# Performance work log

Hardware: AMD Instinct MI355X
Metric: run time of the kernel (lower is better)

The kernel has to match this reference:

```python
import jax, jax.numpy as jnp
import numpy as np

KERNEL_MUL = 2.0
KERNEL_NUM = 5
EPS = 1e-8


def _l2_normalize(x):
    # F.normalize(p=2, dim=-1): x / max(||x||, 1e-12)
    norm = jnp.sqrt(jnp.sum(x * x, axis=-1, keepdims=True))
    return x / jnp.maximum(norm, 1e-12)


def _mmd(source, target):
    n_s = source.shape[0]
    n_t = target.shape[0]
    s = _l2_normalize(source)
    t = _l2_normalize(target)
    total = jnp.concatenate([s, t], axis=0)  # [n, d]
    n = n_s + n_t
    # pairwise squared L2 via norm-expansion trick (avoids [n,n,d] intermediate)
    sq = jnp.sum(total * total, axis=-1)  # [n]
    gram = total @ total.T                # [n, n]
    d2 = jnp.maximum(sq[:, None] + sq[None, :] - 2.0 * gram, 0.0)
    # bandwidth from detached distances (torch uses .data)
    d2_ng = jax.lax.stop_gradient(d2)
    bandwidth = jnp.sum(d2_ng) / (n * n - n) + EPS
    bandwidth = bandwidth / (KERNEL_MUL ** (KERNEL_NUM // 2))
    kernels = jnp.zeros_like(d2)
    for i in range(KERNEL_NUM):
        kernels = kernels + jnp.exp(-d2 / (bandwidth * KERNEL_MUL ** i))
    XX = kernels[:n_s, :n_s]
    YY = kernels[n_s:, n_s:]
    XY = kernels[:n_s, n_s:]
    loss = (jnp.sum(XX) - jnp.trace(XX)) / (n_s * (n_s - 1))
    loss = loss + (jnp.sum(YY) - jnp.trace(YY)) / (n_t * (n_t - 1))
    loss = loss - 2.0 * jnp.sum(XY) / (n_s * n_t)
    return loss


def setup_inputs() -> dict:
    key = jax.random.key(0)
    k1, k2 = jax.random.split(key)
    source = jax.random.normal(k1, (4096, 512), dtype=jnp.float32)
    target = jax.random.normal(k2, (4096, 512), dtype=jnp.float32)
    return {"source": source, "target": target}


def reference(source, target):
    return _mmd(source, target)
```

## Files before the change

### kernel.cpp

```cpp
#include <hip/hip_runtime.h>

#define D 512
#define NS 4096
#define NROWS 8192
#define TILES 32
#define T_SYM 528
#define NBLK_GEMM (2 * T_SYM + TILES * TILES)

typedef __attribute__((ext_vector_type(8))) short bf16x8;
typedef __attribute__((ext_vector_type(4))) float f32x4;

__device__ __forceinline__ unsigned short f2bf(float f) {
  unsigned int u = __float_as_uint(f);
  u += 0x7fffu + ((u >> 16) & 1u);
  return (unsigned short)(u >> 16);
}
__device__ __forceinline__ float bf2f(unsigned short h) {
  return __uint_as_float(((unsigned int)h) << 16);
}
__device__ __forceinline__ void gload_lds16(const void* g, void* l) {
  __builtin_amdgcn_global_load_lds(
      (const __attribute__((address_space(1))) unsigned int*)g,
      (__attribute__((address_space(3))) unsigned int*)l, 16, 0, 0);
}

__global__ __launch_bounds__(256) void k_rownorm(const float* __restrict__ src,
                                                 const float* __restrict__ tgt,
                                                 float* __restrict__ sq,
                                                 unsigned short* __restrict__ hi,
                                                 unsigned short* __restrict__ lo,
                                                 float* __restrict__ colsum) {
  int t = threadIdx.x, w = t >> 6, l = t & 63;
  float csum[8] = {0.f, 0.f, 0.f, 0.f, 0.f, 0.f, 0.f, 0.f};
  for (int i = 0; i < 8; ++i) {
    int r = blockIdx.x * 32 + w * 8 + i;
    const float* p = (r < NS) ? (src + (size_t)r * D) : (tgt + (size_t)(r - NS) * D);
    float4 v0 = *(const float4*)(p + l * 8);
    float4 v1 = *(const float4*)(p + l * 8 + 4);
    float x[8] = {v0.x, v0.y, v0.z, v0.w, v1.x, v1.y, v1.z, v1.w};
    float s = 0.f;
    #pragma unroll
    for (int j = 0; j < 8; ++j) s += x[j] * x[j];
    #pragma unroll
    for (int off = 1; off < 64; off <<= 1) s += __shfl_xor(s, off);
    float iv = 1.0f / fmaxf(sqrtf(s), 1e-12f);
    if (l == 0) sq[r] = s * iv * iv;
    unsigned short hs[8], ls[8];
    #pragma unroll
    for (int j = 0; j < 8; ++j) {
      float xn = x[j] * iv;
      unsigned short h = f2bf(xn);
      hs[j] = h;
      ls[j] = f2bf(xn - bf2f(h));
      csum[j] += xn;
    }
    *(uint4*)&hi[(size_t)r * D + l * 8] = *(uint4*)hs;
    *(uint4*)&lo[(size_t)r * D + l * 8] = *(uint4*)ls;
  }
  __shared__ float cs[4][512];
  #pragma unroll
  for (int j = 0; j < 8; ++j) cs[w][l * 8 + j] = csum[j];
  __syncthreads();
  for (int c = t; c < 512; c += 256)
    atomicAdd(&colsum[c], cs[0][c] + cs[1][c] + cs[2][c] + cs[3][c]);
}

__global__ __launch_bounds__(256) void k_prep(const float* __restrict__ sq,
                                              const float* __restrict__ colsum,
                                              float* __restrict__ na) {
  int t = threadIdx.x;
  double ssq = 0.0;
  for (int i = t; i < NROWS; i += 256) ssq += (double)sq[i];
  double ss2 = 0.0;
  for (int c = t; c < D; c += 256) { double v = (double)colsum[c]; ss2 += v * v; }
  #pragma unroll
  for (int off = 32; off; off >>= 1) {
    ssq += __shfl_down(ssq, off);
    ss2 += __shfl_down(ss2, off);
  }
  __shared__ double l1[4], l2[4];
  if ((t & 63) == 0) { l1[t >> 6] = ssq; l2[t >> 6] = ss2; }
  __syncthreads();
  if (t == 0) {
    double SSQ = l1[0] + l1[1] + l1[2] + l1[3];
    double SS2 = l2[0] + l2[1] + l2[2] + l2[3];
    double n = (double)NROWS;
    double sum_d2 = 2.0 * n * SSQ - 2.0 * SS2;
    double bw = sum_d2 / (n * n - n) + 1e-8;
    bw = bw * 0.25;
    const double LOG2E = 1.4426950408889634;
    na[0] = (float)(-LOG2E / (bw * 16.0));
  }
}

__global__ __launch_bounds__(256) void k_gemm(const unsigned short* __restrict__ hi,
                                              const unsigned short* __restrict__ lo,
                                              const float* __restrict__ sq,
                                              const float* __restrict__ na,
                                              double* __restrict__ part) {
  __shared__ unsigned short lds[2 * 16384];
  __shared__ double red[4];

  int bid0 = blockIdx.x;
  int bid = (bid0 & 7) * (NBLK_GEMM / 8) + (bid0 >> 3);
  int type, bi, bj;
  float wgt = 1.f;
  if (bid < 2 * T_SYM) {
    type = (bid >= T_SYM);
    int idx = bid - type * T_SYM;
    bi = 0;
    while (idx >= TILES - bi) { idx -= TILES - bi; ++bi; }
    bj = bi + idx;
    wgt = (bi == bj) ? 1.f : 2.f;
  } else {
    type = 2;
    int rem = bid - 2 * T_SYM;
    bi = rem >> 5;
    bj = rem & 31;
  }
  int offA = (type == 1) ? NS : 0;
  int offB = (type == 0) ? 0 : NS;

  int t = threadIdx.x;
  int w = t >> 6, l = t & 63;
  int wr = w >> 1, wc = w & 1;
  int fr = l & 15, fk = l >> 4;

  const unsigned short* sarr = (w & 1) ? lo : hi;
  int rbase = ((w < 2) ? (offA + bi * 128) : (offB + bj * 128)) + (l >> 2);
  int gswz = ((l & 3) ^ ((l >> 3) & 3)) * 8;
  const unsigned short* gbase = sarr + (size_t)rbase * D + gswz;

  int rsw = (fr >> 1) & 3;
  int aoff = (wr * 64 + fr) * 32 + (fk ^ rsw) * 8;
  int boff = 8192 + (wc * 64 + fr) * 32 + (fk ^ rsw) * 8;

  f32x4 acc[4][4];
  f32x4 zero = {0.f, 0.f, 0.f, 0.f};
  #pragma unroll
  for (int m = 0; m < 4; ++m)
    #pragma unroll
    for (int n = 0; n < 4; ++n) acc[m][n] = zero;

  #pragma unroll
  for (int c = 0; c < 8; ++c)
    gload_lds16(gbase + (size_t)c * 16 * D, &lds[w * 4096 + c * 512]);
  __syncthreads();

  int cur = 0;
  for (int kt = 0; kt < D / 32; ++kt) {
    int nxt = cur ^ 16384;
    if (kt < D / 32 - 1) {
      #pragma unroll
      for (int c = 0; c < 8; ++c)
        gload_lds16(gbase + (size_t)c * 16 * D + (kt + 1) * 32, &lds[nxt + w * 4096 + c * 512]);
    }
    bf16x8 ah[4], al[4], bh[4], bl[4];
    #pragma unroll
    for (int m = 0; m < 4; ++m) {
      ah[m] = *(const bf16x8*)&lds[cur + aoff + m * 512];
      al[m] = *(const bf16x8*)&lds[cur + 4096 + aoff + m * 512];
    }
    #pragma unroll
    for (int n = 0; n < 4; ++n) {
      bh[n] = *(const bf16x8*)&lds[cur + boff + n * 512];
      bl[n] = *(const bf16x8*)&lds[cur + 12288 + boff + n * 512];
    }
    __builtin_amdgcn_s_setprio(1);
    #pragma unroll
    for (int m = 0; m < 4; ++m)
      #pragma unroll
      for (int n = 0; n < 4; ++n) {
        acc[m][n] = __builtin_amdgcn_mfma_f32_16x16x32_bf16(ah[m], bh[n], acc[m][n], 0, 0, 0);
        acc[m][n] = __builtin_amdgcn_mfma_f32_16x16x32_bf16(ah[m], bl[n], acc[m][n], 0, 0, 0);
        acc[m][n] = __builtin_amdgcn_mfma_f32_16x16x32_bf16(al[m], bh[n], acc[m][n], 0, 0, 0);
      }
    __builtin_amdgcn_s_setprio(0);
    __syncthreads();
    cur = nxt;
  }

  float na4 = na[0];
  int gi = offA + bi * 128 + wr * 64;
  int gj = offB + bj * 128 + wc * 64;
  float sqa[4][4], sqb[4];
  #pragma unroll
  for (int m = 0; m < 4; ++m)
    #pragma unroll
    for (int j = 0; j < 4; ++j) sqa[m][j] = sq[gi + m * 16 + fk * 4 + j];
  #pragma unroll
  for (int n = 0; n < 4; ++n) sqb[n] = sq[gj + n * 16 + fr];

  double local = 0.0;
  #pragma unroll
  for (int m = 0; m < 4; ++m)
    #pragma unroll
    for (int n = 0; n < 4; ++n) {
      float fs = 0.f;
      #pragma unroll
      for (int j = 0; j < 4; ++j) {
        float d2 = fmaxf(fmaf(-2.f, acc[m][n][j], sqa[m][j] + sqb[n]), 0.f);
        float u = __builtin_amdgcn_exp2f(d2 * na4);
        float u2 = u * u, u4 = u2 * u2, u8 = u4 * u4, u16 = u8 * u8;
        fs += (u + u2) + (u4 + u8) + u16;
      }
      local += (double)fs;
    }
  local *= (double)wgt;
  #pragma unroll
  for (int off = 32; off; off >>= 1) local += __shfl_down(local, off);
  if (l == 0) red[w] = local;
  __syncthreads();
  if (t == 0) part[bid] = red[0] + red[1] + red[2] + red[3];
}

__global__ __launch_bounds__(256) void k_final(const double* __restrict__ part,
                                               float* __restrict__ out) {
  int t = threadIdx.x;
  double a0 = 0.0, a1 = 0.0, a2 = 0.0;
  for (int i = t; i < T_SYM; i += 256) a0 += part[i];
  for (int i = t; i < T_SYM; i += 256) a1 += part[T_SYM + i];
  for (int i = t; i < TILES * TILES; i += 256) a2 += part[2 * T_SYM + i];
  #pragma unroll
  for (int off = 32; off; off >>= 1) {
    a0 += __shfl_down(a0, off);
    a1 += __shfl_down(a1, off);
    a2 += __shfl_down(a2, off);
  }
  __shared__ double r0[4], r1[4], r2[4];
  if ((t & 63) == 0) { r0[t >> 6] = a0; r1[t >> 6] = a1; r2[t >> 6] = a2; }
  __syncthreads();
  if (t == 0) {
    double A0 = r0[0] + r0[1] + r0[2] + r0[3];
    double A1 = r1[0] + r1[1] + r1[2] + r1[3];
    double A2 = r2[0] + r2[1] + r2[2] + r2[3];
    double ns = (double)NS;
    double loss = (A0 - 5.0 * ns) / (ns * (ns - 1.0))
                + (A1 - 5.0 * ns) / (ns * (ns - 1.0))
                - 2.0 * A2 / (ns * ns);
    out[0] = (float)loss;
  }
}

extern "C" void kernel_launch(void* const* d_in, const int* in_sizes, int n_in,
                              void* d_out, int out_size, void* d_ws, size_t ws_size,
                              hipStream_t stream) {
  (void)in_sizes; (void)n_in; (void)out_size; (void)ws_size;
  const float* src = (const float*)d_in[0];
  const float* tgt = (const float*)d_in[1];
  float* out = (float*)d_out;
  char* ws = (char*)d_ws;

  double*         part   = (double*)(ws);
  float*          sq     = (float*)(ws + 0x8000);
  float*          colsum = (float*)(ws + 0x10000);
  float*          na     = (float*)(ws + 0x11000);
  unsigned short* hi     = (unsigned short*)(ws + 0x100000);
  unsigned short* lo     = (unsigned short*)(ws + 0x900000);

  hipMemsetAsync(colsum, 0, 512 * sizeof(float), stream);
  hipLaunchKernelGGL(k_rownorm, dim3(256), dim3(256), 0, stream, src, tgt, sq, hi, lo, colsum);
  hipLaunchKernelGGL(k_prep, dim3(1), dim3(256), 0, stream, sq, colsum, na);
  hipLaunchKernelGGL(k_gemm, dim3(NBLK_GEMM), dim3(256), 0, stream, hi, lo, sq, na, part);
  hipLaunchKernelGGL(k_final, dim3(1), dim3(256), 0, stream, part, out);
}
```

Baseline: 216.4 us.

## Enlarge GEMM tiles, add triple-buffered LDS pipeline, fuse final reduction via atomics

The distance GEMM moves from 128x128 tiles with 256 threads and double buffering to 128x256 tiles with 512 threads, a three-stage LDS pipeline driven by explicit vmcnt waits, and raw barriers. Symmetric blocks now use per-element upper-triangle weights instead of whole-tile weights. The final reduction kernel is removed: blocks atomically add into per-type doubles, and the last block, found with a ticket counter, writes the loss. The column-sum atomics and memset are replaced by per-block partials reduced in the prep kernel. The kernel sum now calls exp2 five times instead of using the squaring chain, which adds transcendental work in the epilogue. The larger tiles also waste some compute on the lower halves of diagonal tiles.

```diff
diff --git a/kernel.cpp b/kernel.cpp
--- a/kernel.cpp
+++ b/kernel.cpp
@@ -3,9 +3,9 @@
 #define D 512
 #define NS 4096
 #define NROWS 8192
-#define TILES 32
-#define T_SYM 528
-#define NBLK_GEMM (2 * T_SYM + TILES * TILES)
+#define NB_XX 272
+#define NB_GEMM (2 * NB_XX + 512)
+#define LDSS 24576
 
 typedef __attribute__((ext_vector_type(8))) short bf16x8;
 typedef __attribute__((ext_vector_type(4))) float f32x4;
@@ -23,17 +23,18 @@
       (const __attribute__((address_space(1))) unsigned int*)g,
       (__attribute__((address_space(3))) unsigned int*)l, 16, 0, 0);
 }
-
-__global__ __launch_bounds__(256) void k_rownorm(const float* __restrict__ src,
-                                                 const float* __restrict__ tgt,
-                                                 float* __restrict__ sq,
-                                                 unsigned short* __restrict__ hi,
-                                                 unsigned short* __restrict__ lo,
-                                                 float* __restrict__ colsum) {
+#define WAITV(N) asm volatile("s_waitcnt vmcnt(" #N ")" ::: "memory")
+
+__global__ __launch_bounds__(512) void k_pre(const float* __restrict__ src,
+                                             const float* __restrict__ tgt,
+                                             float* __restrict__ sq,
+                                             unsigned short* __restrict__ hi,
+                                             unsigned short* __restrict__ lo,
+                                             float* __restrict__ Spart) {
   int t = threadIdx.x, w = t >> 6, l = t & 63;
   float csum[8] = {0.f, 0.f, 0.f, 0.f, 0.f, 0.f, 0.f, 0.f};
-  for (int i = 0; i < 8; ++i) {
-    int r = blockIdx.x * 32 + w * 8 + i;
+  for (int i = 0; i < 16; ++i) {
+    int r = blockIdx.x * 128 + w * 16 + i;
     const float* p = (r < NS) ? (src + (size_t)r * D) : (tgt + (size_t)(r - NS) * D);
     float4 v0 = *(const float4*)(p + l * 8);
     float4 v1 = *(const float4*)(p + l * 8 + 4);
@@ -57,79 +58,100 @@
     *(uint4*)&hi[(size_t)r * D + l * 8] = *(uint4*)hs;
     *(uint4*)&lo[(size_t)r * D + l * 8] = *(uint4*)ls;
   }
-  __shared__ float cs[4][512];
+  __shared__ float cs[8][512];
   #pragma unroll
   for (int j = 0; j < 8; ++j) cs[w][l * 8 + j] = csum[j];
   __syncthreads();
-  for (int c = t; c < 512; c += 256)
-    atomicAdd(&colsum[c], cs[0][c] + cs[1][c] + cs[2][c] + cs[3][c]);
-}
-
-__global__ __launch_bounds__(256) void k_prep(const float* __restrict__ sq,
-                                              const float* __restrict__ colsum,
-                                              float* __restrict__ na) {
+  float a = 0.f;
+  #pragma unroll
+  for (int ww = 0; ww < 8; ++ww) a += cs[ww][t];
+  Spart[blockIdx.x * 512 + t] = a;
+}
+
+__global__ __launch_bounds__(512) void k_prep(const float* __restrict__ sq,
+                                              const float* __restrict__ Spart,
+                                              float* __restrict__ na,
+                                              double* __restrict__ dsum,
+                                              unsigned int* __restrict__ cnt) {
   int t = threadIdx.x;
   double ssq = 0.0;
-  for (int i = t; i < NROWS; i += 256) ssq += (double)sq[i];
-  double ss2 = 0.0;
-  for (int c = t; c < D; c += 256) { double v = (double)colsum[c]; ss2 += v * v; }
+  for (int i = t; i < NROWS; i += 512) ssq += (double)sq[i];
+  double cssum = 0.0;
+  for (int b = 0; b < 64; ++b) cssum += (double)Spart[b * 512 + t];
+  double ss2 = cssum * cssum;
   #pragma unroll
   for (int off = 32; off; off >>= 1) {
     ssq += __shfl_down(ssq, off);
     ss2 += __shfl_down(ss2, off);
   }
-  __shared__ double l1[4], l2[4];
+  __shared__ double l1[8], l2[8];
   if ((t & 63) == 0) { l1[t >> 6] = ssq; l2[t >> 6] = ss2; }
   __syncthreads();
   if (t == 0) {
-    double SSQ = l1[0] + l1[1] + l1[2] + l1[3];
-    double SS2 = l2[0] + l2[1] + l2[2] + l2[3];
+    double SSQ = 0.0, SS2 = 0.0;
+    #pragma unroll
+    for (int i = 0; i < 8; ++i) { SSQ += l1[i]; SS2 += l2[i]; }
     double n = (double)NROWS;
     double sum_d2 = 2.0 * n * SSQ - 2.0 * SS2;
     double bw = sum_d2 / (n * n - n) + 1e-8;
     bw = bw * 0.25;
     const double LOG2E = 1.4426950408889634;
-    na[0] = (float)(-LOG2E / (bw * 16.0));
-  }
-}
-
-__global__ __launch_bounds__(256) void k_gemm(const unsigned short* __restrict__ hi,
-                                              const unsigned short* __restrict__ lo,
-                                              const float* __restrict__ sq,
-                                              const float* __restrict__ na,
-                                              double* __restrict__ part) {
-  __shared__ unsigned short lds[2 * 16384];
-  __shared__ double red[4];
+    #pragma unroll
+    for (int m = 0; m < 5; ++m) na[m] = (float)(-LOG2E / (bw * (double)(1 << m)));
+    dsum[0] = 0.0; dsum[1] = 0.0; dsum[2] = 0.0;
+    cnt[0] = 0u;
+  }
+}
+
+__global__ __launch_bounds__(512, 2) void k_gemm(const unsigned short* __restrict__ hi,
+                                                 const unsigned short* __restrict__ lo,
+                                                 const float* __restrict__ sq,
+                                                 const float* __restrict__ na,
+                                                 double* __restrict__ dsum,
+                                                 unsigned int* __restrict__ cnt,
+                                                 float* __restrict__ out) {
+  __shared__ unsigned short lds[3 * LDSS];
+  __shared__ double red[8];
 
   int bid0 = blockIdx.x;
-  int bid = (bid0 & 7) * (NBLK_GEMM / 8) + (bid0 >> 3);
-  int type, bi, bj;
-  float wgt = 1.f;
-  if (bid < 2 * T_SYM) {
-    type = (bid >= T_SYM);
-    int idx = bid - type * T_SYM;
-    bi = 0;
-    while (idx >= TILES - bi) { idx -= TILES - bi; ++bi; }
-    bj = bi + idx;
-    wgt = (bi == bj) ? 1.f : 2.f;
+  int bid = (bid0 & 7) * (NB_GEMM / 8) + (bid0 >> 3);
+  int type, bi, c2;
+  if (bid < 2 * NB_XX) {
+    type = (bid >= NB_XX);
+    int idx = bid - type * NB_XX;
+    int b = 0;
+    while (idx >= 16 - (b >> 1)) { idx -= 16 - (b >> 1); ++b; }
+    bi = b;
+    c2 = (b >> 1) + idx;
   } else {
     type = 2;
-    int rem = bid - 2 * T_SYM;
-    bi = rem >> 5;
-    bj = rem & 31;
+    int rem = bid - 2 * NB_XX;
+    bi = rem >> 4;
+    c2 = rem & 15;
   }
   int offA = (type == 1) ? NS : 0;
   int offB = (type == 0) ? 0 : NS;
+  bool sym = (type < 2);
 
   int t = threadIdx.x;
   int w = t >> 6, l = t & 63;
-  int wr = w >> 1, wc = w & 1;
+  int wr = w >> 2, wc = w & 3;
   int fr = l & 15, fk = l >> 4;
 
-  const unsigned short* sarr = (w & 1) ? lo : hi;
-  int rbase = ((w < 2) ? (offA + bi * 128) : (offB + bj * 128)) + (l >> 2);
-  int gswz = ((l & 3) ^ ((l >> 3) & 3)) * 8;
-  const unsigned short* gbase = sarr + (size_t)rbase * D + gswz;
+  const unsigned short* gsrc[6];
+  int ldsoff[6];
+  #pragma unroll
+  for (int c = 0; c < 6; ++c) {
+    int r = w * 6 + c;
+    int isB = (r >= 16);
+    int isLo = isB ? (r >= 32) : (r >= 8);
+    int rr = isB ? ((r - 16) & 15) : (r & 7);
+    int rowbase = isB ? (offB + c2 * 256 + rr * 16) : (offA + bi * 128 + rr * 16);
+    const unsigned short* arr = isLo ? lo : hi;
+    int gswz = ((l & 3) ^ ((l >> 3) & 3)) * 8;
+    gsrc[c] = arr + (size_t)(rowbase + (l >> 2)) * D + gswz;
+    ldsoff[c] = r * 512;
+  }
 
   int rsw = (fr >> 1) & 3;
   int aoff = (wr * 64 + fr) * 32 + (fk ^ rsw) * 8;
@@ -143,28 +165,31 @@
     for (int n = 0; n < 4; ++n) acc[m][n] = zero;
 
   #pragma unroll
-  for (int c = 0; c < 8; ++c)
-    gload_lds16(gbase + (size_t)c * 16 * D, &lds[w * 4096 + c * 512]);
-  __syncthreads();
-
-  int cur = 0;
-  for (int kt = 0; kt < D / 32; ++kt) {
-    int nxt = cur ^ 16384;
-    if (kt < D / 32 - 1) {
+  for (int c = 0; c < 6; ++c) gload_lds16(gsrc[c], &lds[ldsoff[c]]);
+  #pragma unroll
+  for (int c = 0; c < 6; ++c) gload_lds16(gsrc[c] + 32, &lds[LDSS + ldsoff[c]]);
+
+  unsigned int b0 = 0, b1 = LDSS, b2 = 2 * LDSS;
+  for (int kt = 0; kt < 16; ++kt) {
+    if (kt < 15) { WAITV(6); } else { WAITV(0); }
+    __builtin_amdgcn_s_barrier();
+    __builtin_amdgcn_sched_barrier(0);
+
+    bf16x8 ah[4], al[4], bh[4], bl[4];
+    #pragma unroll
+    for (int m = 0; m < 4; ++m) {
+      ah[m] = *(const bf16x8*)&lds[b0 + aoff + m * 512];
+      al[m] = *(const bf16x8*)&lds[b0 + 4096 + aoff + m * 512];
+    }
+    #pragma unroll
+    for (int n = 0; n < 4; ++n) {
+      bh[n] = *(const bf16x8*)&lds[b0 + boff + n * 512];
+      bl[n] = *(const bf16x8*)&lds[b0 + 8192 + boff + n * 512];
+    }
+    if (kt < 14) {
       #pragma unroll
-      for (int c = 0; c < 8; ++c)
-        gload_lds16(gbase + (size_t)c * 16 * D + (kt + 1) * 32, &lds[nxt + w * 4096 + c * 512]);
-    }
-    bf16x8 ah[4], al[4], bh[4], bl[4];
-    #pragma unroll
-    for (int m = 0; m < 4; ++m) {
-      ah[m] = *(const bf16x8*)&lds[cur + aoff + m * 512];
-      al[m] = *(const bf16x8*)&lds[cur + 4096 + aoff + m * 512];
-    }
-    #pragma unroll
-    for (int n = 0; n < 4; ++n) {
-      bh[n] = *(const bf16x8*)&lds[cur + boff + n * 512];
-      bl[n] = *(const bf16x8*)&lds[cur + 12288 + boff + n * 512];
+      for (int c = 0; c < 6; ++c)
+        gload_lds16(gsrc[c] + (kt + 2) * 32, &lds[b2 + ldsoff[c]]);
     }
     __builtin_amdgcn_s_setprio(1);
     #pragma unroll
@@ -176,69 +201,59 @@
         acc[m][n] = __builtin_amdgcn_mfma_f32_16x16x32_bf16(al[m], bh[n], acc[m][n], 0, 0, 0);
       }
     __builtin_amdgcn_s_setprio(0);
-    __syncthreads();
-    cur = nxt;
-  }
-
-  float na4 = na[0];
-  int gi = offA + bi * 128 + wr * 64;
-  int gj = offB + bj * 128 + wc * 64;
+    unsigned int tmp = b0; b0 = b1; b1 = b2; b2 = tmp;
+  }
+
+  float nam[5];
+  #pragma unroll
+  for (int m2 = 0; m2 < 5; ++m2) nam[m2] = na[m2];
+  int giL0 = bi * 128 + wr * 64;
+  int gjL0 = c2 * 256 + wc * 64;
   float sqa[4][4], sqb[4];
   #pragma unroll
   for (int m = 0; m < 4; ++m)
     #pragma unroll
-    for (int j = 0; j < 4; ++j) sqa[m][j] = sq[gi + m * 16 + fk * 4 + j];
-  #pragma unroll
-  for (int n = 0; n < 4; ++n) sqb[n] = sq[gj + n * 16 + fr];
+    for (int j = 0; j < 4; ++j) sqa[m][j] = sq[offA + giL0 + m * 16 + fk * 4 + j];
+  #pragma unroll
+  for (int n = 0; n < 4; ++n) sqb[n] = sq[offB + gjL0 + n * 16 + fr];
 
   double local = 0.0;
   #pragma unroll
   for (int m = 0; m < 4; ++m)
     #pragma unroll
     for (int n = 0; n < 4; ++n) {
-      float fs = 0.f;
+      int gjL = gjL0 + n * 16 + fr;
       #pragma unroll
       for (int j = 0; j < 4; ++j) {
+        int giL = giL0 + m * 16 + fk * 4 + j;
         float d2 = fmaxf(fmaf(-2.f, acc[m][n][j], sqa[m][j] + sqb[n]), 0.f);
-        float u = __builtin_amdgcn_exp2f(d2 * na4);
-        float u2 = u * u, u4 = u2 * u2, u8 = u4 * u4, u16 = u8 * u8;
-        fs += (u + u2) + (u4 + u8) + u16;
+        float kv = 0.f;
+        #pragma unroll
+        for (int m2 = 0; m2 < 5; ++m2) kv += __builtin_amdgcn_exp2f(d2 * nam[m2]);
+        float wf = sym ? ((gjL > giL) ? 2.f : ((gjL == giL) ? 1.f : 0.f)) : 1.f;
+        local += (double)(wf * kv);
       }
-      local += (double)fs;
-    }
-  local *= (double)wgt;
+    }
   #pragma unroll
   for (int off = 32; off; off >>= 1) local += __shfl_down(local, off);
   if (l == 0) red[w] = local;
   __syncthreads();
-  if (t == 0) part[bid] = red[0] + red[1] + red[2] + red[3];
-}
-
-__global__ __launch_bounds__(256) void k_final(const double* __restrict__ part,
-                                               float* __restrict__ out) {
-  int t = threadIdx.x;
-  double a0 = 0.0, a1 = 0.0, a2 = 0.0;
-  for (int i = t; i < T_SYM; i += 256) a0 += part[i];
-  for (int i = t; i < T_SYM; i += 256) a1 += part[T_SYM + i];
-  for (int i = t; i < TILES * TILES; i += 256) a2 += part[2 * T_SYM + i];
-  #pragma unroll
-  for (int off = 32; off; off >>= 1) {
-    a0 += __shfl_down(a0, off);
-    a1 += __shfl_down(a1, off);
-    a2 += __shfl_down(a2, off);
-  }
-  __shared__ double r0[4], r1[4], r2[4];
-  if ((t & 63) == 0) { r0[t >> 6] = a0; r1[t >> 6] = a1; r2[t >> 6] = a2; }
-  __syncthreads();
   if (t == 0) {
-    double A0 = r0[0] + r0[1] + r0[2] + r0[3];
-    double A1 = r1[0] + r1[1] + r1[2] + r1[3];
-    double A2 = r2[0] + r2[1] + r2[2] + r2[3];
-    double ns = (double)NS;
-    double loss = (A0 - 5.0 * ns) / (ns * (ns - 1.0))
-                + (A1 - 5.0 * ns) / (ns * (ns - 1.0))
-                - 2.0 * A2 / (ns * ns);
-    out[0] = (float)loss;
+    double bsum = 0.0;
+    #pragma unroll
+    for (int i = 0; i < 8; ++i) bsum += red[i];
+    atomicAdd(&dsum[type], bsum);
+    __threadfence();
+    unsigned int ticket = atomicAdd(cnt, 1u);
+    if (ticket == NB_GEMM - 1) {
+      __threadfence();
+      double A0 = dsum[0], A1 = dsum[1], A2 = dsum[2];
+      double ns = (double)NS;
+      double loss = (A0 - 5.0 * ns) / (ns * (ns - 1.0))
+                  + (A1 - 5.0 * ns) / (ns * (ns - 1.0))
+                  - 2.0 * A2 / (ns * ns);
+      out[0] = (float)loss;
+    }
   }
 }
 
@@ -251,16 +266,15 @@
   float* out = (float*)d_out;
   char* ws = (char*)d_ws;
 
-  double*         part   = (double*)(ws);
-  float*          sq     = (float*)(ws + 0x8000);
-  float*          colsum = (float*)(ws + 0x10000);
-  float*          na     = (float*)(ws + 0x11000);
-  unsigned short* hi     = (unsigned short*)(ws + 0x100000);
-  unsigned short* lo     = (unsigned short*)(ws + 0x900000);
-
-  hipMemsetAsync(colsum, 0, 512 * sizeof(float), stream);
-  hipLaunchKernelGGL(k_rownorm, dim3(256), dim3(256), 0, stream, src, tgt, sq, hi, lo, colsum);
-  hipLaunchKernelGGL(k_prep, dim3(1), dim3(256), 0, stream, sq, colsum, na);
-  hipLaunchKernelGGL(k_gemm, dim3(NBLK_GEMM), dim3(256), 0, stream, hi, lo, sq, na, part);
-  hipLaunchKernelGGL(k_final, dim3(1), dim3(256), 0, stream, part, out);
-}
+  float*          sq    = (float*)(ws);
+  float*          Spart = (float*)(ws + 0x8000);
+  float*          na    = (float*)(ws + 0x28000);
+  double*         dsum  = (double*)(ws + 0x28040);
+  unsigned int*   cnt   = (unsigned int*)(ws + 0x28080);
+  unsigned short* hi    = (unsigned short*)(ws + 0x100000);
+  unsigned short* lo    = (unsigned short*)(ws + 0x900000);
+
+  hipLaunchKernelGGL(k_pre, dim3(64), dim3(512), 0, stream, src, tgt, sq, hi, lo, Spart);
+  hipLaunchKernelGGL(k_prep, dim3(1), dim3(512), 0, stream, sq, Spart, na, dsum, cnt);
+  hipLaunchKernelGGL(k_gemm, dim3(NB_GEMM), dim3(512), 0, stream, hi, lo, sq, na, dsum, cnt, out);
+}
```

After: 232.4 us. 1.07x slower.

## Switch split-bf16 Gram to split-int8 MFMA and fuse prep/final reductions

Applied to the files above, without the earlier changes.

Replaces the hi/lo bf16 split GEMM with a fixed-point int8 hi/lo split: each normalized value is quantized to 14 fractional bits and split into two int8 halves. Four int8 16x16x64 MFMAs per tile pair are accumulated exactly in int32 and recombined in double. The prep kernel is folded into the row-normalization kernel through a last-block ticket, and the final reduction is folded into the GEMM through atomic double sums and a completion counter, which cuts the launch count from four kernels to two. The epilogue now computes five separate exp2 calls instead of the squaring chain, which adds transcendental work and changes precision characteristics through the fixed-point quantization.

```diff
diff --git a/kernel.cpp b/kernel.cpp
--- a/kernel.cpp
+++ b/kernel.cpp
@@ -5,35 +5,29 @@
 #define NROWS 8192
 #define TILES 32
 #define T_SYM 528
-#define NBLK_GEMM (2 * T_SYM + TILES * TILES)
-
-typedef __attribute__((ext_vector_type(8))) short bf16x8;
-typedef __attribute__((ext_vector_type(4))) float f32x4;
-
-__device__ __forceinline__ unsigned short f2bf(float f) {
-  unsigned int u = __float_as_uint(f);
-  u += 0x7fffu + ((u >> 16) & 1u);
-  return (unsigned short)(u >> 16);
-}
-__device__ __forceinline__ float bf2f(unsigned short h) {
-  return __uint_as_float(((unsigned int)h) << 16);
-}
+#define NBLK (2 * T_SYM + TILES * TILES)
+#define LA_OFF 0x400000u
+
+typedef __attribute__((ext_vector_type(4))) int i32x4;
+
 __device__ __forceinline__ void gload_lds16(const void* g, void* l) {
   __builtin_amdgcn_global_load_lds(
       (const __attribute__((address_space(1))) unsigned int*)g,
       (__attribute__((address_space(3))) unsigned int*)l, 16, 0, 0);
 }
 
-__global__ __launch_bounds__(256) void k_rownorm(const float* __restrict__ src,
-                                                 const float* __restrict__ tgt,
-                                                 float* __restrict__ sq,
-                                                 unsigned short* __restrict__ hi,
-                                                 unsigned short* __restrict__ lo,
-                                                 float* __restrict__ colsum) {
+__global__ __launch_bounds__(512) void k_pre(const float* __restrict__ src,
+                                             const float* __restrict__ tgt,
+                                             float* __restrict__ sq,
+                                             signed char* __restrict__ ha,
+                                             signed char* __restrict__ la,
+                                             float* __restrict__ Spart,
+                                             float* __restrict__ na,
+                                             unsigned int* __restrict__ pcnt) {
   int t = threadIdx.x, w = t >> 6, l = t & 63;
   float csum[8] = {0.f, 0.f, 0.f, 0.f, 0.f, 0.f, 0.f, 0.f};
-  for (int i = 0; i < 8; ++i) {
-    int r = blockIdx.x * 32 + w * 8 + i;
+  for (int i = 0; i < 16; ++i) {
+    int r = blockIdx.x * 128 + w * 16 + i;
     const float* p = (r < NS) ? (src + (size_t)r * D) : (tgt + (size_t)(r - NS) * D);
     float4 v0 = *(const float4*)(p + l * 8);
     float4 v1 = *(const float4*)(p + l * 8 + 4);
@@ -44,65 +38,79 @@
     #pragma unroll
     for (int off = 1; off < 64; off <<= 1) s += __shfl_xor(s, off);
     float iv = 1.0f / fmaxf(sqrtf(s), 1e-12f);
-    if (l == 0) sq[r] = s * iv * iv;
-    unsigned short hs[8], ls[8];
+    signed char hs[8], ls[8];
+    int sxx = 0;
     #pragma unroll
     for (int j = 0; j < 8; ++j) {
       float xn = x[j] * iv;
-      unsigned short h = f2bf(xn);
-      hs[j] = h;
-      ls[j] = f2bf(xn - bf2f(h));
+      int X = __float2int_rn(xn * 16384.f);
+      int h = (X + 128) >> 8;
+      int lo = X - (h << 8);
+      hs[j] = (signed char)h;
+      ls[j] = (signed char)lo;
+      sxx += X * X;
       csum[j] += xn;
     }
-    *(uint4*)&hi[(size_t)r * D + l * 8] = *(uint4*)hs;
-    *(uint4*)&lo[(size_t)r * D + l * 8] = *(uint4*)ls;
-  }
-  __shared__ float cs[4][512];
+    #pragma unroll
+    for (int off = 1; off < 64; off <<= 1) sxx += __shfl_xor(sxx, off);
+    if (l == 0) sq[r] = (float)((double)sxx * (1.0 / 268435456.0));
+    *(uint2*)&ha[(size_t)r * 512 + l * 8] = *(uint2*)hs;
+    *(uint2*)&la[(size_t)r * 512 + l * 8] = *(uint2*)ls;
+  }
+  __shared__ float cs[8][512];
   #pragma unroll
   for (int j = 0; j < 8; ++j) cs[w][l * 8 + j] = csum[j];
   __syncthreads();
-  for (int c = t; c < 512; c += 256)
-    atomicAdd(&colsum[c], cs[0][c] + cs[1][c] + cs[2][c] + cs[3][c]);
-}
-
-__global__ __launch_bounds__(256) void k_prep(const float* __restrict__ sq,
-                                              const float* __restrict__ colsum,
-                                              float* __restrict__ na) {
-  int t = threadIdx.x;
-  double ssq = 0.0;
-  for (int i = t; i < NROWS; i += 256) ssq += (double)sq[i];
-  double ss2 = 0.0;
-  for (int c = t; c < D; c += 256) { double v = (double)colsum[c]; ss2 += v * v; }
-  #pragma unroll
-  for (int off = 32; off; off >>= 1) {
-    ssq += __shfl_down(ssq, off);
-    ss2 += __shfl_down(ss2, off);
-  }
-  __shared__ double l1[4], l2[4];
-  if ((t & 63) == 0) { l1[t >> 6] = ssq; l2[t >> 6] = ss2; }
-  __syncthreads();
-  if (t == 0) {
-    double SSQ = l1[0] + l1[1] + l1[2] + l1[3];
-    double SS2 = l2[0] + l2[1] + l2[2] + l2[3];
-    double n = (double)NROWS;
-    double sum_d2 = 2.0 * n * SSQ - 2.0 * SS2;
-    double bw = sum_d2 / (n * n - n) + 1e-8;
-    bw = bw * 0.25;
-    const double LOG2E = 1.4426950408889634;
-    na[0] = (float)(-LOG2E / (bw * 16.0));
-  }
-}
-
-__global__ __launch_bounds__(256) void k_gemm(const unsigned short* __restrict__ hi,
-                                              const unsigned short* __restrict__ lo,
-                                              const float* __restrict__ sq,
-                                              const float* __restrict__ na,
-                                              double* __restrict__ part) {
-  __shared__ unsigned short lds[2 * 16384];
+  float a = 0.f;
+  #pragma unroll
+  for (int ww = 0; ww < 8; ++ww) a += cs[ww][t];
+  Spart[blockIdx.x * 512 + t] = a;
+
+  __threadfence();
+  __shared__ unsigned int lastFlag;
+  if (t == 0) lastFlag = (atomicAdd(pcnt, 1u) == 63u) ? 1u : 0u;
+  __syncthreads();
+  if (lastFlag) {
+    __threadfence();
+    double ssq = 0.0;
+    for (int i = t; i < NROWS; i += 512) ssq += (double)sq[i];
+    double cssum = 0.0;
+    for (int b = 0; b < 64; ++b) cssum += (double)Spart[b * 512 + t];
+    double ss2 = cssum * cssum;
+    #pragma unroll
+    for (int off = 32; off; off >>= 1) {
+      ssq += __shfl_down(ssq, off);
+      ss2 += __shfl_down(ss2, off);
+    }
+    __shared__ double l1[8], l2[8];
+    if ((t & 63) == 0) { l1[t >> 6] = ssq; l2[t >> 6] = ss2; }
+    __syncthreads();
+    if (t == 0) {
+      double SSQ = 0.0, SS2 = 0.0;
+      #pragma unroll
+      for (int i = 0; i < 8; ++i) { SSQ += l1[i]; SS2 += l2[i]; }
+      double n = (double)NROWS;
+      double sum_d2 = 2.0 * n * SSQ - 2.0 * SS2;
+      double bw = sum_d2 / (n * n - n) + 1e-8;
+      bw = bw * 0.25;
+      const double LOG2E = 1.4426950408889634;
+      #pragma unroll
+      for (int m = 0; m < 5; ++m) na[m] = (float)(-LOG2E / (bw * (double)(1 << m)));
+    }
+  }
+}
+
+__global__ __launch_bounds__(256, 2) void k_gemm(const signed char* __restrict__ ha,
+                                                 const float* __restrict__ sq,
+                                                 const float* __restrict__ na,
+                                                 double* __restrict__ dsum,
+                                                 unsigned int* __restrict__ ccnt,
+                                                 float* __restrict__ out) {
+  __shared__ signed char lds[2 * 32768];
   __shared__ double red[4];
 
   int bid0 = blockIdx.x;
-  int bid = (bid0 & 7) * (NBLK_GEMM / 8) + (bid0 >> 3);
+  int bid = (bid0 & 7) * (NBLK / 8) + (bid0 >> 3);
   int type, bi, bj;
   float wgt = 1.f;
   if (bid < 2 * T_SYM) {
@@ -126,61 +134,71 @@
   int wr = w >> 1, wc = w & 1;
   int fr = l & 15, fk = l >> 4;
 
-  const unsigned short* sarr = (w & 1) ? lo : hi;
-  int rbase = ((w < 2) ? (offA + bi * 128) : (offB + bj * 128)) + (l >> 2);
-  int gswz = ((l & 3) ^ ((l >> 3) & 3)) * 8;
-  const unsigned short* gbase = sarr + (size_t)rbase * D + gswz;
+  int gswz = ((l & 3) ^ ((l >> 3) & 3)) * 16;
+  unsigned baseA = (unsigned)((offA + bi * 128 + (l >> 2)) * 512) + (unsigned)gswz;
+  unsigned baseB = (unsigned)((offB + bj * 128 + (l >> 2)) * 512) + (unsigned)gswz;
+  unsigned srcoff[8];
+  #pragma unroll
+  for (int c = 0; c < 8; ++c) {
+    int r = w * 8 + c;
+    unsigned base = (r >= 16) ? baseB : baseA;
+    unsigned lofix = ((r & 8) ? LA_OFF : 0u) + (unsigned)((r & 7) * 8192);
+    srcoff[c] = base + lofix;
+  }
+  int ldsw = w * 8192;
 
   int rsw = (fr >> 1) & 3;
-  int aoff = (wr * 64 + fr) * 32 + (fk ^ rsw) * 8;
-  int boff = 8192 + (wc * 64 + fr) * 32 + (fk ^ rsw) * 8;
-
-  f32x4 acc[4][4];
-  f32x4 zero = {0.f, 0.f, 0.f, 0.f};
+  int aOff = wr * 4096 + fr * 64 + ((fk ^ rsw) * 16);
+  int bOff = 16384 + wc * 4096 + fr * 64 + ((fk ^ rsw) * 16);
+
+  i32x4 acc1[4][4], acc2[4][4], acc3[4][4];
+  i32x4 izero = {0, 0, 0, 0};
   #pragma unroll
   for (int m = 0; m < 4; ++m)
     #pragma unroll
-    for (int n = 0; n < 4; ++n) acc[m][n] = zero;
+    for (int n = 0; n < 4; ++n) { acc1[m][n] = izero; acc2[m][n] = izero; acc3[m][n] = izero; }
 
   #pragma unroll
   for (int c = 0; c < 8; ++c)
-    gload_lds16(gbase + (size_t)c * 16 * D, &lds[w * 4096 + c * 512]);
-  __syncthreads();
-
-  int cur = 0;
-  for (int kt = 0; kt < D / 32; ++kt) {
-    int nxt = cur ^ 16384;
-    if (kt < D / 32 - 1) {
+    gload_lds16(ha + (size_t)srcoff[c], &lds[ldsw + c * 1024]);
+  __syncthreads();
+
+  int bb = 0;
+  for (int kt = 0; kt < 8; ++kt) {
+    if (kt < 7) {
       #pragma unroll
       for (int c = 0; c < 8; ++c)
-        gload_lds16(gbase + (size_t)c * 16 * D + (kt + 1) * 32, &lds[nxt + w * 4096 + c * 512]);
-    }
-    bf16x8 ah[4], al[4], bh[4], bl[4];
-    #pragma unroll
-    for (int m = 0; m < 4; ++m) {
-      ah[m] = *(const bf16x8*)&lds[cur + aoff + m * 512];
-      al[m] = *(const bf16x8*)&lds[cur + 4096 + aoff + m * 512];
-    }
-    #pragma unroll
-    for (int n = 0; n < 4; ++n) {
-      bh[n] = *(const bf16x8*)&lds[cur + boff + n * 512];
-      bl[n] = *(const bf16x8*)&lds[cur + 12288 + boff + n * 512];
+        gload_lds16(ha + (size_t)(srcoff[c] + (unsigned)(kt + 1) * 64u),
+                    &lds[(bb ^ 32768) + ldsw + c * 1024]);
     }
     __builtin_amdgcn_s_setprio(1);
     #pragma unroll
-    for (int m = 0; m < 4; ++m)
+    for (int mp = 0; mp < 2; ++mp) {
+      i32x4 A0h = *(const i32x4*)&lds[bb + aOff + (mp * 2) * 1024];
+      i32x4 A1h = *(const i32x4*)&lds[bb + aOff + (mp * 2 + 1) * 1024];
+      i32x4 A0l = *(const i32x4*)&lds[bb + 8192 + aOff + (mp * 2) * 1024];
+      i32x4 A1l = *(const i32x4*)&lds[bb + 8192 + aOff + (mp * 2 + 1) * 1024];
       #pragma unroll
       for (int n = 0; n < 4; ++n) {
-        acc[m][n] = __builtin_amdgcn_mfma_f32_16x16x32_bf16(ah[m], bh[n], acc[m][n], 0, 0, 0);
-        acc[m][n] = __builtin_amdgcn_mfma_f32_16x16x32_bf16(ah[m], bl[n], acc[m][n], 0, 0, 0);
-        acc[m][n] = __builtin_amdgcn_mfma_f32_16x16x32_bf16(al[m], bh[n], acc[m][n], 0, 0, 0);
+        i32x4 Bh = *(const i32x4*)&lds[bb + bOff + n * 1024];
+        i32x4 Bl = *(const i32x4*)&lds[bb + 8192 + bOff + n * 1024];
+        int m0 = mp * 2, m1 = mp * 2 + 1;
+        acc1[m0][n] = __builtin_amdgcn_mfma_i32_16x16x64_i8(A0h, Bh, acc1[m0][n], 0, 0, 0);
+        acc2[m0][n] = __builtin_amdgcn_mfma_i32_16x16x64_i8(A0h, Bl, acc2[m0][n], 0, 0, 0);
+        acc2[m0][n] = __builtin_amdgcn_mfma_i32_16x16x64_i8(A0l, Bh, acc2[m0][n], 0, 0, 0);
+        acc3[m0][n] = __builtin_amdgcn_mfma_i32_16x16x64_i8(A0l, Bl, acc3[m0][n], 0, 0, 0);
+        acc1[m1][n] = __builtin_amdgcn_mfma_i32_16x16x64_i8(A1h, Bh, acc1[m1][n], 0, 0, 0);
+        acc2[m1][n] = __builtin_amdgcn_mfma_i32_16x16x64_i8(A1h, Bl, acc2[m1][n], 0, 0, 0);
+        acc2[m1][n] = __builtin_amdgcn_mfma_i32_16x16x64_i8(A1l, Bh, acc2[m1][n], 0, 0, 0);
+        acc3[m1][n] = __builtin_amdgcn_mfma_i32_16x16x64_i8(A1l, Bl, acc3[m1][n], 0, 0, 0);
       }
+    }
     __builtin_amdgcn_s_setprio(0);
     __syncthreads();
-    cur = nxt;
-  }
-
-  float na4 = na[0];
+    bb ^= 32768;
+  }
+
+  float nam0 = na[0], nam1 = na[1], nam2 = na[2], nam3 = na[3], nam4 = na[4];
   int gi = offA + bi * 128 + wr * 64;
   int gj = offB + bj * 128 + wc * 64;
   float sqa[4][4], sqb[4];
@@ -195,50 +213,37 @@
   #pragma unroll
   for (int m = 0; m < 4; ++m)
     #pragma unroll
-    for (int n = 0; n < 4; ++n) {
-      float fs = 0.f;
+    for (int n = 0; n < 4; ++n)
       #pragma unroll
       for (int j = 0; j < 4; ++j) {
-        float d2 = fmaxf(fmaf(-2.f, acc[m][n][j], sqa[m][j] + sqb[n]), 0.f);
-        float u = __builtin_amdgcn_exp2f(d2 * na4);
-        float u2 = u * u, u4 = u2 * u2, u8 = u4 * u4, u16 = u8 * u8;
-        fs += (u + u2) + (u4 + u8) + u16;
+        double tt = 65536.0 * (double)acc1[m][n][j] + 256.0 * (double)acc2[m][n][j]
+                  + (double)acc3[m][n][j];
+        double d2d = (double)sqa[m][j] + (double)sqb[n] - tt * 7.450580596923828e-9;
+        float d2v = fmaxf((float)d2d, 0.f);
+        float kv = __builtin_amdgcn_exp2f(d2v * nam0) + __builtin_amdgcn_exp2f(d2v * nam1)
+                 + __builtin_amdgcn_exp2f(d2v * nam2) + __builtin_amdgcn_exp2f(d2v * nam3)
+                 + __builtin_amdgcn_exp2f(d2v * nam4);
+        local += (double)kv;
       }
-      local += (double)fs;
-    }
   local *= (double)wgt;
   #pragma unroll
   for (int off = 32; off; off >>= 1) local += __shfl_down(local, off);
   if (l == 0) red[w] = local;
   __syncthreads();
-  if (t == 0) part[bid] = red[0] + red[1] + red[2] + red[3];
-}
-
-__global__ __launch_bounds__(256) void k_final(const double* __restrict__ part,
-                                               float* __restrict__ out) {
-  int t = threadIdx.x;
-  double a0 = 0.0, a1 = 0.0, a2 = 0.0;
-  for (int i = t; i < T_SYM; i += 256) a0 += part[i];
-  for (int i = t; i < T_SYM; i += 256) a1 += part[T_SYM + i];
-  for (int i = t; i < TILES * TILES; i += 256) a2 += part[2 * T_SYM + i];
-  #pragma unroll
-  for (int off = 32; off; off >>= 1) {
-    a0 += __shfl_down(a0, off);
-    a1 += __shfl_down(a1, off);
-    a2 += __shfl_down(a2, off);
-  }
-  __shared__ double r0[4], r1[4], r2[4];
-  if ((t & 63) == 0) { r0[t >> 6] = a0; r1[t >> 6] = a1; r2[t >> 6] = a2; }
-  __syncthreads();
   if (t == 0) {
-    double A0 = r0[0] + r0[1] + r0[2] + r0[3];
-    double A1 = r1[0] + r1[1] + r1[2] + r1[3];
-    double A2 = r2[0] + r2[1] + r2[2] + r2[3];
-    double ns = (double)NS;
-    double loss = (A0 - 5.0 * ns) / (ns * (ns - 1.0))
-                + (A1 - 5.0 * ns) / (ns * (ns - 1.0))
-                - 2.0 * A2 / (ns * ns);
-    out[0] = (float)loss;
+    double bsum = red[0] + red[1] + red[2] + red[3];
+    atomicAdd(&dsum[type], bsum);
+    __threadfence();
+    unsigned int ticket = atomicAdd(ccnt, 1u);
+    if (ticket == NBLK - 1) {
+      __threadfence();
+      double A0 = dsum[0], A1 = dsum[1], A2 = dsum[2];
+      double ns = (double)NS;
+      double loss = (A0 - 5.0 * ns) / (ns * (ns - 1.0))
+                  + (A1 - 5.0 * ns) / (ns * (ns - 1.0))
+                  - 2.0 * A2 / (ns * ns);
+      out[0] = (float)loss;
+    }
   }
 }
 
@@ -251,16 +256,16 @@
   float* out = (float*)d_out;
   char* ws = (char*)d_ws;
 
-  double*         part   = (double*)(ws);
-  float*          sq     = (float*)(ws + 0x8000);
-  float*          colsum = (float*)(ws + 0x10000);
-  float*          na     = (float*)(ws + 0x11000);
-  unsigned short* hi     = (unsigned short*)(ws + 0x100000);
-  unsigned short* lo     = (unsigned short*)(ws + 0x900000);
-
-  hipMemsetAsync(colsum, 0, 512 * sizeof(float), stream);
-  hipLaunchKernelGGL(k_rownorm, dim3(256), dim3(256), 0, stream, src, tgt, sq, hi, lo, colsum);
-  hipLaunchKernelGGL(k_prep, dim3(1), dim3(256), 0, stream, sq, colsum, na);
-  hipLaunchKernelGGL(k_gemm, dim3(NBLK_GEMM), dim3(256), 0, stream, hi, lo, sq, na, part);
-  hipLaunchKernelGGL(k_final, dim3(1), dim3(256), 0, stream, part, out);
-}
+  float*        sq    = (float*)(ws);
+  float*        Spart = (float*)(ws + 0x8000);
+  float*        na    = (float*)(ws + 0x28000);
+  double*       dsum  = (double*)(ws + 0x28040);
+  unsigned int* pcnt  = (unsigned int*)(ws + 0x28058);
+  unsigned int* ccnt  = (unsigned int*)(ws + 0x2805C);
+  signed char*  ha    = (signed char*)(ws + 0x100000);
+  signed char*  la    = (signed char*)(ws + 0x500000);
+
+  hipMemsetAsync(ws + 0x28040, 0, 0x20, stream);
+  hipLaunchKernelGGL(k_pre, dim3(64), dim3(512), 0, stream, src, tgt, sq, ha, la, Spart, na, pcnt);
+  hipLaunchKernelGGL(k_gemm, dim3(NBLK), dim3(256), 0, stream, ha, sq, na, dsum, ccnt, out);
+}
```

Result: slower. 280.5 us (+29.6%).
